# Kernel tuning notes

Hardware: AMD Instinct MI355X
Metric: run time of the kernel (lower is better)

The kernel has to match this reference:

```python
import jax, jax.numpy as jnp
import numpy as np
from jax import lax

DN = ('NHWC', 'HWIO', 'NHWC')

def conv2d_same(x, W, b):
    y = lax.conv_general_dilated(x, W, window_strides=(1, 1), padding='SAME', dimension_numbers=DN)
    return y + b

def maxpool2(x):
    # 2x2 max pool, stride 2, SAME padding (NHWC)
    return lax.reduce_window(x, -jnp.inf, lax.max, (1, 2, 2, 1), (1, 2, 2, 1), 'SAME')

def setup_inputs() -> dict:
    key = jax.random.key(0)
    ks = jax.random.split(key, 6)
    B, H, W, C = 8, 64, 64, 256
    s = 0.05
    return {
        'x': jax.random.normal(ks[0], (B, H, W, C), jnp.float32),
        'Wf': jax.random.normal(ks[1], (3, 3, C, C // 8), jnp.float32) * s,
        'bf': jnp.zeros((C // 8,), jnp.float32),
        'Wg': jax.random.normal(ks[2], (3, 3, C, C // 8), jnp.float32) * s,
        'bg': jnp.zeros((C // 8,), jnp.float32),
        'Wh': jax.random.normal(ks[3], (3, 3, C, C // 2), jnp.float32) * s,
        'bh': jnp.zeros((C // 2,), jnp.float32),
        'Wo': jax.random.normal(ks[4], (1, 1, C // 2, C), jnp.float32) * s,
        'bo': jnp.zeros((C,), jnp.float32),
        'gate': jnp.ones((1,), jnp.float32),
    }

def reference(x, Wf, bf, Wg, bg, Wh, bh, Wo, bo, gate):
    B, H, W, C = x.shape
    f = maxpool2(conv2d_same(x, Wf, bf))            # [B, H/2, W/2, C//8] keys
    g = conv2d_same(x, Wg, bg)                       # [B, H, W, C//8]     queries
    h = maxpool2(conv2d_same(x, Wh, bh))            # [B, H/2, W/2, C//2] values
    N, M = H * W, (H // 2) * (W // 2)
    gq = g.reshape(B, N, C // 8)
    fk = f.reshape(B, M, C // 8)
    hv = h.reshape(B, M, C // 2)
    attn = jax.nn.softmax(jnp.einsum('bnd,bmd->bnm', gq, fk), axis=-1)  # [B, N, M]
    wo = jnp.einsum('bnm,bmv->bnv', attn, hv).reshape(B, H, W, C // 2)
    out = conv2d_same(wo, Wo, bo)                    # [B, H, W, C]
    return x + gate[0] * out
```

## Files before the change

kernel.cpp:

```cpp
#include <hip/hip_runtime.h>
#include <hip/hip_fp16.h>

constexpr int B_  = 8;
constexpr int H_  = 64;
constexpr int W_  = 64;
constexpr int C_  = 256;
constexpr int CG_ = 32;
constexpr int CH_ = 128;
constexpr int NQ_ = 4096;
constexpr int NM_ = 1024;
constexpr int XP_ = 66;

constexpr int GP_ = 1048576;
constexpr int HP_ = 4194304;

constexpr int NWPK_ = 12 * 9 * 8 * 64 * 8;
constexpr int NWOK_ = 16 * 4 * 64 * 8;
constexpr int NXC_  = B_ * XP_ * XP_ * 32;

typedef __attribute__((ext_vector_type(8))) _Float16 half8;
typedef __attribute__((ext_vector_type(4))) _Float16 half4;
typedef __attribute__((ext_vector_type(4))) float    f32x4;

__global__ void prep_all_k(const float* __restrict__ X,
                           const float* __restrict__ Wg, const float* __restrict__ Wf,
                           const float* __restrict__ Wh, const float* __restrict__ Wo,
                           const float* __restrict__ bg, const float* __restrict__ bf,
                           const float* __restrict__ bh,
                           _Float16* __restrict__ Xpad, _Float16* __restrict__ Wpk,
                           _Float16* __restrict__ Wok, float* __restrict__ bc) {
    int i = blockIdx.x * 256 + threadIdx.x;
    if (i < NXC_) {
        int c8 = i & 31;
        int px = i >> 5;
        int xx = px % XP_;
        int t  = px / XP_;
        int yy = t % XP_;
        int b  = t / XP_;
        half8 v = (half8)(_Float16)0.f;
        if (yy >= 1 && yy <= 64 && xx >= 1 && xx <= 64) {
            const float* s = X + (((size_t)(b * 64 + yy - 1) * 64) + (xx - 1)) * 256 + c8 * 8;
            float4 a  = *reinterpret_cast<const float4*>(s);
            float4 b2 = *reinterpret_cast<const float4*>(s + 4);
            v[0] = (_Float16)a.x;  v[1] = (_Float16)a.y;
            v[2] = (_Float16)a.z;  v[3] = (_Float16)a.w;
            v[4] = (_Float16)b2.x; v[5] = (_Float16)b2.y;
            v[6] = (_Float16)b2.z; v[7] = (_Float16)b2.w;
        }
        *reinterpret_cast<half8*>(Xpad + (size_t)i * 8) = v;
        return;
    }
    int iw = i - NXC_;
    if (iw < NWPK_) {
        int j    = iw & 7;
        int lane = (iw >> 3) & 63;
        int ks   = (iw >> 9) & 7;
        int tap  = (iw >> 12) % 9;
        int co16 = iw / 36864;
        int co = co16 * 16 + (lane & 15);
        int kk = tap * 256 + ks * 32 + (lane >> 4) * 8 + j;
        float v;
        if (co < 32)      v = Wg[(size_t)kk * 32  + co];
        else if (co < 64) v = Wf[(size_t)kk * 32  + (co - 32)];
        else              v = Wh[(size_t)kk * 128 + (co - 64)];
        Wpk[iw] = (_Float16)v;
        return;
    }
    int i2 = iw - NWPK_;
    if (i2 < NWOK_) {
        int j    = i2 & 7;
        int lane = (i2 >> 3) & 63;
        int ks   = (i2 >> 9) & 3;
        int co16 = i2 >> 11;
        int co = co16 * 16 + (lane & 15);
        int k  = ks * 32 + (lane >> 4) * 8 + j;
        Wok[i2] = (_Float16)Wo[(size_t)k * 256 + co];
        return;
    }
    int co = i2 - NWOK_;
    if (co < 192)
        bc[co] = (co < 32) ? bg[co] : (co < 64) ? bf[co - 32] : bh[co - 64];
}

__global__ __launch_bounds__(256, 8) void conv_mfma_k(
        const _Float16* __restrict__ Xpad, const _Float16* __restrict__ Wpk,
        const float* __restrict__ bc,
        _Float16* __restrict__ gpart, _Float16* __restrict__ fpart,
        _Float16* __restrict__ hpart) {
    __shared__ char lds[34 * 512];
    int bid = blockIdx.x;
    int lg  = (bid & 7) * 384 + (bid >> 3);
    int ky  = lg % 3;
    int t   = lg / 3;
    int xh  = t & 1;
    int y   = (t >> 1) & 63;
    int b   = t >> 7;
    int tid = threadIdx.x;
    int nw  = tid >> 6;
    int l   = tid & 63;
    int lr  = l & 15;
    int lk  = l >> 4;

    {
        const float4* src = reinterpret_cast<const float4*>(
            Xpad + (((size_t)(b * XP_ + y + ky) * XP_) + xh * 32) * 256);
        for (int c = tid; c < 34 * 32; c += 256) {
            int q = c >> 5;
            float4 v = src[c];
            *reinterpret_cast<float4*>(lds + ((c * 16) ^ ((q & 7) << 4))) = v;
        }
    }
    __syncthreads();

    f32x4 acc[2][3];
#pragma unroll
    for (int mi = 0; mi < 2; ++mi)
#pragma unroll
        for (int nj = 0; nj < 3; ++nj) acc[mi][nj] = (f32x4)0.f;

    int tap0 = ky * 3;
#pragma unroll
    for (int st = 0; st < 24; ++st) {
        int kx = st >> 3, ks = st & 7;
        const _Float16* wp = Wpk +
            ((((size_t)(nw * 3) * 9 + tap0 + kx) * 8 + ks) * 64 + l) * 8;
        half8 w0 = *reinterpret_cast<const half8*>(wp);
        half8 w1 = *reinterpret_cast<const half8*>(wp + 36864);
        half8 w2 = *reinterpret_cast<const half8*>(wp + 73728);
        half8 af[2];
#pragma unroll
        for (int mi = 0; mi < 2; ++mi) {
            int q  = mi * 16 + lr + kx;
            int ad = (q * 512 + ks * 64 + lk * 16) ^ ((q & 7) << 4);
            af[mi] = *reinterpret_cast<const half8*>(lds + ad);
        }
#pragma unroll
        for (int mi = 0; mi < 2; ++mi)
            acc[mi][0] = __builtin_amdgcn_mfma_f32_16x16x32_f16(af[mi], w0, acc[mi][0], 0, 0, 0);
#pragma unroll
        for (int mi = 0; mi < 2; ++mi)
            acc[mi][1] = __builtin_amdgcn_mfma_f32_16x16x32_f16(af[mi], w1, acc[mi][1], 0, 0, 0);
#pragma unroll
        for (int mi = 0; mi < 2; ++mi)
            acc[mi][2] = __builtin_amdgcn_mfma_f32_16x16x32_f16(af[mi], w2, acc[mi][2], 0, 0, 0);
    }

    int pixbase = (b * 64 + y) * 64 + xh * 32;
    bool addb = (ky == 1);
#pragma unroll
    for (int nj = 0; nj < 3; ++nj) {
        int co = nw * 48 + nj * 16 + lr;
        float bias = addb ? bc[co] : 0.f;
#pragma unroll
        for (int mi = 0; mi < 2; ++mi) {
#pragma unroll
            for (int r = 0; r < 4; ++r) {
                int px = mi * 16 + lk * 4 + r;
                float v = acc[mi][nj][r] + bias;
                size_t pix = pixbase + px;
                if (co < 32)
                    gpart[(size_t)ky * GP_ + pix * 32 + co] = (_Float16)(v * 1.44269504f);
                else if (co < 64)
                    fpart[(size_t)ky * GP_ + pix * 32 + (co - 32)] = (_Float16)v;
                else
                    hpart[(size_t)ky * HP_ + pix * 128 + (co - 64)] = (_Float16)v;
            }
        }
    }
}

__global__ __launch_bounds__(256) void pools_k(const _Float16* __restrict__ fp,
                                               const _Float16* __restrict__ hp,
                                               _Float16* __restrict__ Kf,
                                               _Float16* __restrict__ Vt) {
    __shared__ float t[32][33];
    int blk = blockIdx.x;
    int tid = threadIdx.x;
    if (blk < 1024) {
        int i = blk * 256 + tid;
        int c = i & 31;
        int t2 = i >> 5;
        int px = t2 & 31;
        int py = (t2 >> 5) & 31;
        int b  = t2 >> 10;
        size_t base = (((size_t)(b * 64 + py * 2)) * 64 + px * 2) * 32 + c;
        const _Float16* p1 = fp + GP_;
        const _Float16* p2 = fp + 2 * GP_;
        auto val = [&](size_t o) { return (float)fp[o] + (float)p1[o] + (float)p2[o]; };
        float v = fmaxf(fmaxf(val(base), val(base + 32)),
                        fmaxf(val(base + 64 * 32), val(base + 64 * 32 + 32)));
        Kf[i] = (_Float16)v;
        return;
    }
    int bx = blk - 1024;
    int b  = bx >> 7;
    int kt = (bx >> 2) & 31;
    int ct = bx & 3;
    const _Float16* p1 = hp + HP_;
    const _Float16* p2 = hp + 2 * (size_t)HP_;
#pragma unroll
    for (int i = 0; i < 4; ++i) {
        int e = tid + i * 256;
        int px = e >> 5, c = e & 31;
        size_t base = (((size_t)(b * 64 + kt * 2) * 64) + px * 2) * 128 + ct * 32 + c;
        auto val = [&](size_t o) { return (float)hp[o] + (float)p1[o] + (float)p2[o]; };
        float v = fmaxf(fmaxf(val(base), val(base + 128)),
                        fmaxf(val(base + 64 * 128), val(base + 64 * 128 + 128)));
        t[px][c] = v;
    }
    __syncthreads();
#pragma unroll
    for (int i = 0; i < 4; ++i) {
        int e = tid + i * 256;
        int c = e >> 5, px = e & 31;
        Vt[((size_t)b * 128 + ct * 32 + c) * 1024 + kt * 32 + px] = (_Float16)t[px][c];
    }
}

constexpr int PP_ = 72;

__global__ __launch_bounds__(256, 2) void attn_flash_k(
        const _Float16* __restrict__ Qp,
        const _Float16* __restrict__ Kf,
        const _Float16* __restrict__ Vt,
        _Float16* __restrict__ wo) {
    __shared__ _Float16 plds[4][16][PP_];
    __shared__ _Float16 vlds[2][8192];
    int bb  = blockIdx.x >> 6;
    int qt  = blockIdx.x & 63;
    int wid = threadIdx.x >> 6;
    int l   = threadIdx.x & 63;
    int lr  = l & 15;
    int lg  = l >> 4;
    int qbase = qt * 64 + wid * 16;

    const _Float16* gp = Qp + ((size_t)bb * NQ_ + qbase + lr) * 32 + lg * 8;
    half8 bq = *reinterpret_cast<const half8*>(gp);
    bq = bq + *reinterpret_cast<const half8*>(gp + GP_);
    bq = bq + *reinterpret_cast<const half8*>(gp + 2 * GP_);

    const _Float16* Kb = Kf + (size_t)bb * NM_ * 32;
    const _Float16* Vb = Vt + (size_t)bb * 128 * NM_;

    int o0  = wid * 4096 + l * 16;
    int vr0 = o0 >> 7;
    int vc  = (o0 >> 4) & 7;
    int vsw = (vr0 & 7) << 4;
    int lsw = (lr & 7) << 4;

    f32x4 acc[8];
#pragma unroll
    for (int vt = 0; vt < 8; ++vt) acc[vt] = (f32x4)0.f;
    float m_run = -1.0e30f;
    float l_lane = 0.f;

    half8 ak0, ak1, ak2, ak3;
    f32x4 s0, s1, s2, s3;
    half4 ph0, ph1, ph2, ph3;
    float4 vst[4];

#define STAGE_LOAD(T)                                                              \
    {   const _Float16* vp = Vb + (size_t)(T) * 64 + (size_t)vr0 * NM_ + vc * 8;   \
        vst[0] = *reinterpret_cast<const float4*>(vp);                             \
        vst[1] = *reinterpret_cast<const float4*>(vp + 8 * NM_);                   \
        vst[2] = *reinterpret_cast<const float4*>(vp + 16 * NM_);                  \
        vst[3] = *reinterpret_cast<const float4*>(vp + 24 * NM_);                  \
    }

#define STAGE_WRITE(BUF)                                                           \
    {   char* vbp = (char*)vlds[BUF] + (o0 ^ vsw);                                 \
        *reinterpret_cast<float4*>(vbp)        = vst[0];                           \
        *reinterpret_cast<float4*>(vbp + 1024) = vst[1];                           \
        *reinterpret_cast<float4*>(vbp + 2048) = vst[2];                           \
        *reinterpret_cast<float4*>(vbp + 3072) = vst[3];                           \
    }

#define LOADK(T)                                                                   \
    {   const _Float16* kp = Kb + (size_t)(T) * 64 * 32;                           \
        ak0 = *reinterpret_cast<const half8*>(kp + (size_t)(lr)      * 32 + lg*8); \
        ak1 = *reinterpret_cast<const half8*>(kp + (size_t)(16 + lr) * 32 + lg*8); \
        ak2 = *reinterpret_cast<const half8*>(kp + (size_t)(32 + lr) * 32 + lg*8); \
        ak3 = *reinterpret_cast<const half8*>(kp + (size_t)(48 + lr) * 32 + lg*8); \
    }

#define QK()                                                                \
    {   __builtin_amdgcn_s_setprio(1);                                      \
        s0 = __builtin_amdgcn_mfma_f32_16x16x32_f16(ak0, bq, (f32x4)0.f, 0, 0, 0); \
        s1 = __builtin_amdgcn_mfma_f32_16x16x32_f16(ak1, bq, (f32x4)0.f, 0, 0, 0); \
        s2 = __builtin_amdgcn_mfma_f32_16x16x32_f16(ak2, bq, (f32x4)0.f, 0, 0, 0); \
        s3 = __builtin_amdgcn_mfma_f32_16x16x32_f16(ak3, bq, (f32x4)0.f, 0, 0, 0); \
        __builtin_amdgcn_s_setprio(0);                                      \
    }

#define SOFTMAX()                                                           \
    {   float lm = fmaxf(fmaxf(fmaxf(s0[0], s0[1]), fmaxf(s0[2], s0[3])),   \
                         fmaxf(fmaxf(s1[0], s1[1]), fmaxf(s1[2], s1[3])));  \
        lm = fmaxf(lm, fmaxf(fmaxf(fmaxf(s2[0], s2[1]), fmaxf(s2[2], s2[3])), \
                             fmaxf(fmaxf(s3[0], s3[1]), fmaxf(s3[2], s3[3])))); \
        if (__any(lm > m_run + 11.0f)) {                                    \
            float mx = lm;                                                  \
            mx = fmaxf(mx, __shfl_xor(mx, 16, 64));                         \
            mx = fmaxf(mx, __shfl_xor(mx, 32, 64));                         \
            float mnew  = fmaxf(m_run, mx);                                 \
            float alpha = exp2f(m_run - mnew);                              \
            l_lane *= alpha;                                                \
            _Pragma("unroll")                                               \
            for (int r = 0; r < 4; ++r) {                                   \
                float ar = __shfl(alpha, 4 * lg + r, 64);                   \
                _Pragma("unroll")                                           \
                for (int vt = 0; vt < 8; ++vt) acc[vt][r] *= ar;            \
            }                                                               \
            m_run = mnew;                                                   \
        }                                                                   \
        float ps = 0.f;                                                     \
        {   float p0 = exp2f(s0[0]-m_run), p1 = exp2f(s0[1]-m_run);         \
            float p2 = exp2f(s0[2]-m_run), p3 = exp2f(s0[3]-m_run);         \
            ps += (p0+p1)+(p2+p3);                                          \
            ph0[0]=(_Float16)p0; ph0[1]=(_Float16)p1;                       \
            ph0[2]=(_Float16)p2; ph0[3]=(_Float16)p3; }                     \
        {   float p0 = exp2f(s1[0]-m_run), p1 = exp2f(s1[1]-m_run);         \
            float p2 = exp2f(s1[2]-m_run), p3 = exp2f(s1[3]-m_run);         \
            ps += (p0+p1)+(p2+p3);                                          \
            ph1[0]=(_Float16)p0; ph1[1]=(_Float16)p1;                       \
            ph1[2]=(_Float16)p2; ph1[3]=(_Float16)p3; }                     \
        {   float p0 = exp2f(s2[0]-m_run), p1 = exp2f(s2[1]-m_run);         \
            float p2 = exp2f(s2[2]-m_run), p3 = exp2f(s2[3]-m_run);         \
            ps += (p0+p1)+(p2+p3);                                          \
            ph2[0]=(_Float16)p0; ph2[1]=(_Float16)p1;                       \
            ph2[2]=(_Float16)p2; ph2[3]=(_Float16)p3; }                     \
        {   float p0 = exp2f(s3[0]-m_run), p1 = exp2f(s3[1]-m_run);         \
            float p2 = exp2f(s3[2]-m_run), p3 = exp2f(s3[3]-m_run);         \
            ps += (p0+p1)+(p2+p3);                                          \
            ph3[0]=(_Float16)p0; ph3[1]=(_Float16)p1;                       \
            ph3[2]=(_Float16)p2; ph3[3]=(_Float16)p3; }                     \
        l_lane += ps;                                                       \
    }

#define WRITEP()                                                            \
    {   *reinterpret_cast<half4*>(&plds[wid][lr][ 0 + 4*lg]) = ph0;         \
        *reinterpret_cast<half4*>(&plds[wid][lr][16 + 4*lg]) = ph1;         \
        *reinterpret_cast<half4*>(&plds[wid][lr][32 + 4*lg]) = ph2;         \
        *reinterpret_cast<half4*>(&plds[wid][lr][48 + 4*lg]) = ph3;         \
    }

#define PV(BUF)                                                             \
    {   half8 ap0 = *reinterpret_cast<const half8*>(&plds[wid][lr][8*lg]);  \
        half8 ap1 = *reinterpret_cast<const half8*>(&plds[wid][lr][32 + 8*lg]); \
        const char* vbp = (const char*)vlds[BUF];                           \
        __builtin_amdgcn_s_setprio(1);                                      \
        _Pragma("unroll")                                                   \
        for (int vt = 0; vt < 8; ++vt) {                                    \
            int ra = (vt * 16 + lr) * 128;                                  \
            half8 bv = *reinterpret_cast<const half8*>(                     \
                vbp + ((ra + lg * 16) ^ lsw));                              \
            acc[vt] = __builtin_amdgcn_mfma_f32_16x16x32_f16(ap0, bv, acc[vt], 0, 0, 0); \
        }                                                                   \
        _Pragma("unroll")                                                   \
        for (int vt = 0; vt < 8; ++vt) {                                    \
            int ra = (vt * 16 + lr) * 128;                                  \
            half8 bv = *reinterpret_cast<const half8*>(                     \
                vbp + ((ra + (4 + lg) * 16) ^ lsw));                        \
            acc[vt] = __builtin_amdgcn_mfma_f32_16x16x32_f16(ap1, bv, acc[vt], 0, 0, 0); \
        }                                                                   \
        __builtin_amdgcn_s_setprio(0);                                      \
    }

    STAGE_LOAD(0);
    STAGE_WRITE(0);
    LOADK(0);
    __syncthreads();
    QK(); SOFTMAX();

    for (int t = 0; t < 16; ++t) {
        if (t < 15) { STAGE_LOAD(t + 1); LOADK(t + 1); }
        WRITEP();
        PV(t & 1);
        if (t < 15) STAGE_WRITE((t + 1) & 1);
        __syncthreads();
        if (t < 15) { QK(); SOFTMAX(); }
    }

#undef STAGE_LOAD
#undef STAGE_WRITE
#undef LOADK
#undef QK
#undef SOFTMAX
#undef WRITEP
#undef PV

    float lsum = l_lane;
    lsum += __shfl_xor(lsum, 16, 64);
    lsum += __shfl_xor(lsum, 32, 64);
    float inv = 1.f / lsum;
#pragma unroll
    for (int r = 0; r < 4; ++r) {
        float ir = __shfl(inv, 4 * lg + r, 64);
        _Float16* orow = wo + ((size_t)bb * NQ_ + qbase + 4 * lg + r) * 128 + lr;
#pragma unroll
        for (int vt = 0; vt < 8; ++vt) orow[vt * 16] = (_Float16)(acc[vt][r] * ir);
    }
}

__global__ __launch_bounds__(256, 2) void conv1x1_mfma_k(
        const _Float16* __restrict__ wo, const _Float16* __restrict__ Wok,
        const float* __restrict__ bo, const float* __restrict__ X,
        const float* __restrict__ gate, float* __restrict__ out) {
    __shared__ char lds[64 * 256];
    int pix0 = blockIdx.x * 64;
    int tid = threadIdx.x;
    int wq = tid >> 6;
    int l  = tid & 63;
    int lr = l & 15;
    int lg = l >> 4;

    {
        const float4* sp = reinterpret_cast<const float4*>(wo + (size_t)pix0 * 128);
#pragma unroll
        for (int j = 0; j < 4; ++j) {
            int c = tid + j * 256;
            int px = c >> 4;
            *reinterpret_cast<float4*>(lds + ((c * 16) ^ ((px & 7) << 4))) = sp[c];
        }
    }
    __syncthreads();

    f32x4 acc[4][4];
#pragma unroll
    for (int mi = 0; mi < 4; ++mi)
#pragma unroll
        for (int nj = 0; nj < 4; ++nj) acc[mi][nj] = (f32x4)0.f;

#pragma unroll
    for (int ks = 0; ks < 4; ++ks) {
        half8 ap[4];
#pragma unroll
        for (int mi = 0; mi < 4; ++mi) {
            int px = mi * 16 + lr;
            int ad = (px * 256 + ks * 64 + lg * 16) ^ ((px & 7) << 4);
            ap[mi] = *reinterpret_cast<const half8*>(lds + ad);
        }
#pragma unroll
        for (int nj = 0; nj < 4; ++nj) {
            int co16 = wq * 4 + nj;
            half8 bv = *reinterpret_cast<const half8*>(
                Wok + (((size_t)co16 * 4 + ks) * 64 + l) * 8);
#pragma unroll
            for (int mi = 0; mi < 4; ++mi)
                acc[mi][nj] = __builtin_amdgcn_mfma_f32_16x16x32_f16(ap[mi], bv, acc[mi][nj], 0, 0, 0);
        }
    }

    float gt = gate[0];
#pragma unroll
    for (int nj = 0; nj < 4; ++nj) {
        int co = wq * 64 + nj * 16 + lr;
        float bias = bo[co];
#pragma unroll
        for (int mi = 0; mi < 4; ++mi) {
#pragma unroll
            for (int r = 0; r < 4; ++r) {
                size_t o = (size_t)(pix0 + mi * 16 + lg * 4 + r) * 256 + co;
                out[o] = X[o] + gt * (acc[mi][nj][r] + bias);
            }
        }
    }
}

extern "C" void kernel_launch(void* const* d_in, const int* in_sizes, int n_in,
                              void* d_out, int out_size, void* d_ws, size_t ws_size,
                              hipStream_t stream) {
    const float* X    = (const float*)d_in[0];
    const float* Wf   = (const float*)d_in[1];
    const float* bf   = (const float*)d_in[2];
    const float* Wg   = (const float*)d_in[3];
    const float* bg   = (const float*)d_in[4];
    const float* Wh   = (const float*)d_in[5];
    const float* bh   = (const float*)d_in[6];
    const float* Wo   = (const float*)d_in[7];
    const float* bo   = (const float*)d_in[8];
    const float* gate = (const float*)d_in[9];
    float* out = (float*)d_out;

    _Float16* gpart = (_Float16*)d_ws;
    _Float16* fpart = gpart + 3 * (size_t)GP_;
    _Float16* hpart = fpart + 3 * (size_t)GP_;
    _Float16* Kf    = hpart + 3 * (size_t)HP_;
    _Float16* Vt    = Kf + 262144;
    _Float16* Wpk   = Vt + 1048576;
    float*    bc    = (float*)(Wpk + 589824);
    _Float16* Wok   = (_Float16*)(bc + 192);
    _Float16* Xpad  = Wok + 32768;
    _Float16* wobuf = hpart;

    int prep_n = NXC_ + NWPK_ + NWOK_ + 192;
    prep_all_k<<<(prep_n + 255) / 256, 256, 0, stream>>>(
        X, Wg, Wf, Wh, Wo, bg, bf, bh, Xpad, Wpk, Wok, bc);
    conv_mfma_k<<<3 * B_ * 64 * 2, 256, 0, stream>>>(Xpad, Wpk, bc, gpart, fpart, hpart);
    pools_k<<<2048, 256, 0, stream>>>(fpart, hpart, Kf, Vt);
    attn_flash_k<<<B_ * 64, 256, 0, stream>>>(gpart, Kf, Vt, wobuf);
    conv1x1_mfma_k<<<(B_ * NQ_) / 64, 256, 0, stream>>>(wobuf, Wok, bo, X, gate, out);
}
```

Baseline: 118.4 us.

## Process full image row per conv block and prefetch next weight fragments

```diff
diff --git a/kernel.cpp b/kernel.cpp
--- a/kernel.cpp
+++ b/kernel.cpp
@@ -82,82 +82,96 @@
         bc[co] = (co < 32) ? bg[co] : (co < 64) ? bf[co - 32] : bh[co - 64];
 }
 
-__global__ __launch_bounds__(256, 8) void conv_mfma_k(
+__global__ __launch_bounds__(256, 4) void conv_mfma_k(
         const _Float16* __restrict__ Xpad, const _Float16* __restrict__ Wpk,
         const float* __restrict__ bc,
         _Float16* __restrict__ gpart, _Float16* __restrict__ fpart,
         _Float16* __restrict__ hpart) {
-    __shared__ char lds[34 * 512];
+    __shared__ char lds[XP_ * 256 * 2];
     int bid = blockIdx.x;
-    int lg  = (bid & 7) * 384 + (bid >> 3);
+    int lg  = (bid & 7) * 192 + (bid >> 3);
     int ky  = lg % 3;
-    int t   = lg / 3;
-    int xh  = t & 1;
-    int y   = (t >> 1) & 63;
-    int b   = t >> 7;
+    int iy  = lg / 3;
+    int b   = iy >> 6;
+    int y   = iy & 63;
     int tid = threadIdx.x;
-    int nw  = tid >> 6;
+    int wid = tid >> 6;
     int l   = tid & 63;
     int lr  = l & 15;
     int lk  = l >> 4;
 
     {
-        const float4* src = reinterpret_cast<const float4*>(
-            Xpad + (((size_t)(b * XP_ + y + ky) * XP_) + xh * 32) * 256);
-        for (int c = tid; c < 34 * 32; c += 256) {
-            int q = c >> 5;
-            float4 v = src[c];
-            *reinterpret_cast<float4*>(lds + ((c * 16) ^ ((q & 7) << 4))) = v;
+        const float4* sp = reinterpret_cast<const float4*>(
+            Xpad + ((size_t)(b * XP_ + y + ky) * XP_) * 256);
+        float4 vst[8];
+#pragma unroll
+        for (int j = 0; j < 8; ++j) vst[j] = sp[tid + j * 256];
+        float4 tl;
+        if (tid < 64) tl = sp[tid + 2048];
+#pragma unroll
+        for (int j = 0; j < 8; ++j) {
+            int c = tid + j * 256; int px = c >> 5;
+            *reinterpret_cast<float4*>(lds + ((c * 16) ^ ((px & 7) << 4))) = vst[j];
+        }
+        if (tid < 64) {
+            int c = tid + 2048; int px = c >> 5;
+            *reinterpret_cast<float4*>(lds + ((c * 16) ^ ((px & 7) << 4))) = tl;
         }
     }
     __syncthreads();
 
-    f32x4 acc[2][3];
-#pragma unroll
-    for (int mi = 0; mi < 2; ++mi)
+    f32x4 acc[4][3];
+#pragma unroll
+    for (int mi = 0; mi < 4; ++mi)
 #pragma unroll
         for (int nj = 0; nj < 3; ++nj) acc[mi][nj] = (f32x4)0.f;
 
+    auto ldw = [&](int tap, int ks, half8& d0, half8& d1, half8& d2) {
+        const _Float16* p = Wpk + ((((size_t)(wid * 3) * 9 + tap) * 8 + ks) * 64 + l) * 8;
+        d0 = *reinterpret_cast<const half8*>(p);
+        d1 = *reinterpret_cast<const half8*>(p + 36864);
+        d2 = *reinterpret_cast<const half8*>(p + 73728);
+    };
+
     int tap0 = ky * 3;
+    half8 b0, b1, b2, n0, n1, n2;
+    ldw(tap0, 0, b0, b1, b2);
 #pragma unroll
     for (int st = 0; st < 24; ++st) {
         int kx = st >> 3, ks = st & 7;
-        const _Float16* wp = Wpk +
-            ((((size_t)(nw * 3) * 9 + tap0 + kx) * 8 + ks) * 64 + l) * 8;
-        half8 w0 = *reinterpret_cast<const half8*>(wp);
-        half8 w1 = *reinterpret_cast<const half8*>(wp + 36864);
-        half8 w2 = *reinterpret_cast<const half8*>(wp + 73728);
-        half8 af[2];
-#pragma unroll
-        for (int mi = 0; mi < 2; ++mi) {
-            int q  = mi * 16 + lr + kx;
-            int ad = (q * 512 + ks * 64 + lk * 16) ^ ((q & 7) << 4);
+        if (st < 23) ldw(tap0 + ((st + 1) >> 3), (st + 1) & 7, n0, n1, n2);
+        half8 af[4];
+#pragma unroll
+        for (int mi = 0; mi < 4; ++mi) {
+            int px = mi * 16 + lr + kx;
+            int ad = (px * 512 + ks * 64 + lk * 16) ^ ((px & 7) << 4);
             af[mi] = *reinterpret_cast<const half8*>(lds + ad);
         }
 #pragma unroll
-        for (int mi = 0; mi < 2; ++mi)
-            acc[mi][0] = __builtin_amdgcn_mfma_f32_16x16x32_f16(af[mi], w0, acc[mi][0], 0, 0, 0);
-#pragma unroll
-        for (int mi = 0; mi < 2; ++mi)
-            acc[mi][1] = __builtin_amdgcn_mfma_f32_16x16x32_f16(af[mi], w1, acc[mi][1], 0, 0, 0);
-#pragma unroll
-        for (int mi = 0; mi < 2; ++mi)
-            acc[mi][2] = __builtin_amdgcn_mfma_f32_16x16x32_f16(af[mi], w2, acc[mi][2], 0, 0, 0);
-    }
-
-    int pixbase = (b * 64 + y) * 64 + xh * 32;
+        for (int mi = 0; mi < 4; ++mi)
+            acc[mi][0] = __builtin_amdgcn_mfma_f32_16x16x32_f16(af[mi], b0, acc[mi][0], 0, 0, 0);
+#pragma unroll
+        for (int mi = 0; mi < 4; ++mi)
+            acc[mi][1] = __builtin_amdgcn_mfma_f32_16x16x32_f16(af[mi], b1, acc[mi][1], 0, 0, 0);
+#pragma unroll
+        for (int mi = 0; mi < 4; ++mi)
+            acc[mi][2] = __builtin_amdgcn_mfma_f32_16x16x32_f16(af[mi], b2, acc[mi][2], 0, 0, 0);
+        b0 = n0; b1 = n1; b2 = n2;
+    }
+
+    int pixbase = (b * 64 + y) * 64;
     bool addb = (ky == 1);
 #pragma unroll
     for (int nj = 0; nj < 3; ++nj) {
-        int co = nw * 48 + nj * 16 + lr;
+        int co = wid * 48 + nj * 16 + lr;
         float bias = addb ? bc[co] : 0.f;
 #pragma unroll
-        for (int mi = 0; mi < 2; ++mi) {
+        for (int mi = 0; mi < 4; ++mi) {
 #pragma unroll
             for (int r = 0; r < 4; ++r) {
-                int px = mi * 16 + lk * 4 + r;
+                int x = mi * 16 + lk * 4 + r;
                 float v = acc[mi][nj][r] + bias;
-                size_t pix = pixbase + px;
+                size_t pix = pixbase + x;
                 if (co < 32)
                     gpart[(size_t)ky * GP_ + pix * 32 + co] = (_Float16)(v * 1.44269504f);
                 else if (co < 64)
@@ -495,7 +509,7 @@
     int prep_n = NXC_ + NWPK_ + NWOK_ + 192;
     prep_all_k<<<(prep_n + 255) / 256, 256, 0, stream>>>(
         X, Wg, Wf, Wh, Wo, bg, bf, bh, Xpad, Wpk, Wok, bc);
-    conv_mfma_k<<<3 * B_ * 64 * 2, 256, 0, stream>>>(Xpad, Wpk, bc, gpart, fpart, hpart);
+    conv_mfma_k<<<3 * B_ * H_, 256, 0, stream>>>(Xpad, Wpk, bc, gpart, fpart, hpart);
     pools_k<<<2048, 256, 0, stream>>>(fpart, hpart, Kf, Vt);
     attn_flash_k<<<B_ * 64, 256, 0, stream>>>(gpart, Kf, Vt, wobuf);
     conv1x1_mfma_k<<<(B_ * NQ_) / 64, 256, 0, stream>>>(wobuf, Wok, bo, X, gate, out);
```

After: 104.2 us (median of 2 runs). -12.0%, faster.

## Switch 3x3 conv to 32x32x16 MFMA over full-row tiles with weight prefetch

Applied to the files above, without the earlier changes.

```diff
diff --git a/kernel.cpp b/kernel.cpp
--- a/kernel.cpp
+++ b/kernel.cpp
@@ -14,13 +14,14 @@
 constexpr int GP_ = 1048576;
 constexpr int HP_ = 4194304;
 
-constexpr int NWPK_ = 12 * 9 * 8 * 64 * 8;
+constexpr int NWPK_ = 6 * 9 * 16 * 64 * 8;
 constexpr int NWOK_ = 16 * 4 * 64 * 8;
 constexpr int NXC_  = B_ * XP_ * XP_ * 32;
 
-typedef __attribute__((ext_vector_type(8))) _Float16 half8;
-typedef __attribute__((ext_vector_type(4))) _Float16 half4;
-typedef __attribute__((ext_vector_type(4))) float    f32x4;
+typedef __attribute__((ext_vector_type(8)))  _Float16 half8;
+typedef __attribute__((ext_vector_type(4)))  _Float16 half4;
+typedef __attribute__((ext_vector_type(4)))  float    f32x4;
+typedef __attribute__((ext_vector_type(16))) float    f32x16;
 
 __global__ void prep_all_k(const float* __restrict__ X,
                            const float* __restrict__ Wg, const float* __restrict__ Wf,
@@ -54,11 +55,11 @@
     if (iw < NWPK_) {
         int j    = iw & 7;
         int lane = (iw >> 3) & 63;
-        int ks   = (iw >> 9) & 7;
-        int tap  = (iw >> 12) % 9;
-        int co16 = iw / 36864;
-        int co = co16 * 16 + (lane & 15);
-        int kk = tap * 256 + ks * 32 + (lane >> 4) * 8 + j;
+        int ks   = (iw >> 9) & 15;
+        int tap  = (iw >> 13) % 9;
+        int co32 = iw / 73728;
+        int co = co32 * 32 + (lane & 31);
+        int kk = tap * 256 + ks * 16 + (lane >> 5) * 8 + j;
         float v;
         if (co < 32)      v = Wg[(size_t)kk * 32  + co];
         else if (co < 64) v = Wf[(size_t)kk * 32  + (co - 32)];
@@ -82,80 +83,82 @@
         bc[co] = (co < 32) ? bg[co] : (co < 64) ? bf[co - 32] : bh[co - 64];
 }
 
-__global__ __launch_bounds__(256, 8) void conv_mfma_k(
+__global__ __launch_bounds__(192, 3) void conv_mfma_k(
         const _Float16* __restrict__ Xpad, const _Float16* __restrict__ Wpk,
         const float* __restrict__ bc,
         _Float16* __restrict__ gpart, _Float16* __restrict__ fpart,
         _Float16* __restrict__ hpart) {
-    __shared__ char lds[34 * 512];
+    __shared__ char lds[XP_ * 256 * 2];
     int bid = blockIdx.x;
-    int lg  = (bid & 7) * 384 + (bid >> 3);
+    int lg  = (bid & 7) * 192 + (bid >> 3);
     int ky  = lg % 3;
-    int t   = lg / 3;
-    int xh  = t & 1;
-    int y   = (t >> 1) & 63;
-    int b   = t >> 7;
+    int iy  = lg / 3;
+    int b   = iy >> 6;
+    int y   = iy & 63;
     int tid = threadIdx.x;
-    int nw  = tid >> 6;
+    int w   = tid >> 6;
     int l   = tid & 63;
-    int lr  = l & 15;
-    int lk  = l >> 4;
+    int l31 = l & 31;
+    int lh  = l >> 5;
 
     {
-        const float4* src = reinterpret_cast<const float4*>(
-            Xpad + (((size_t)(b * XP_ + y + ky) * XP_) + xh * 32) * 256);
-        for (int c = tid; c < 34 * 32; c += 256) {
-            int q = c >> 5;
-            float4 v = src[c];
-            *reinterpret_cast<float4*>(lds + ((c * 16) ^ ((q & 7) << 4))) = v;
+        const float4* sp = reinterpret_cast<const float4*>(
+            Xpad + ((size_t)(b * XP_ + y + ky) * XP_) * 256);
+        for (int c = tid; c < XP_ * 32; c += 192) {
+            int px = c >> 5;
+            float4 v = sp[c];
+            *reinterpret_cast<float4*>(lds + ((c * 16) ^ ((px & 15) << 4))) = v;
         }
     }
     __syncthreads();
 
-    f32x4 acc[2][3];
+    f32x16 acc[2][2];
 #pragma unroll
     for (int mi = 0; mi < 2; ++mi)
 #pragma unroll
-        for (int nj = 0; nj < 3; ++nj) acc[mi][nj] = (f32x4)0.f;
+        for (int nj = 0; nj < 2; ++nj) acc[mi][nj] = (f32x16)0.f;
 
     int tap0 = ky * 3;
-#pragma unroll
-    for (int st = 0; st < 24; ++st) {
-        int kx = st >> 3, ks = st & 7;
-        const _Float16* wp = Wpk +
-            ((((size_t)(nw * 3) * 9 + tap0 + kx) * 8 + ks) * 64 + l) * 8;
-        half8 w0 = *reinterpret_cast<const half8*>(wp);
-        half8 w1 = *reinterpret_cast<const half8*>(wp + 36864);
-        half8 w2 = *reinterpret_cast<const half8*>(wp + 73728);
+    auto ldw = [&](int s, half8& d0, half8& d1) {
+        const _Float16* p = Wpk +
+            ((((size_t)(w * 2) * 9 + tap0 + (s >> 4)) * 16 + (s & 15)) * 64 + l) * 8;
+        d0 = *reinterpret_cast<const half8*>(p);
+        d1 = *reinterpret_cast<const half8*>(p + 73728);
+    };
+
+    half8 b0, b1, n0, n1;
+    ldw(0, b0, b1);
+#pragma unroll
+    for (int st = 0; st < 48; ++st) {
+        int kx = st >> 4, ks = st & 15;
+        if (st < 47) ldw(st + 1, n0, n1);
         half8 af[2];
 #pragma unroll
         for (int mi = 0; mi < 2; ++mi) {
-            int q  = mi * 16 + lr + kx;
-            int ad = (q * 512 + ks * 64 + lk * 16) ^ ((q & 7) << 4);
+            int px = mi * 32 + l31 + kx;
+            int ad = (px * 512 + ks * 32 + lh * 16) ^ ((px & 15) << 4);
             af[mi] = *reinterpret_cast<const half8*>(lds + ad);
         }
 #pragma unroll
         for (int mi = 0; mi < 2; ++mi)
-            acc[mi][0] = __builtin_amdgcn_mfma_f32_16x16x32_f16(af[mi], w0, acc[mi][0], 0, 0, 0);
+            acc[mi][0] = __builtin_amdgcn_mfma_f32_32x32x16_f16(af[mi], b0, acc[mi][0], 0, 0, 0);
 #pragma unroll
         for (int mi = 0; mi < 2; ++mi)
-            acc[mi][1] = __builtin_amdgcn_mfma_f32_16x16x32_f16(af[mi], w1, acc[mi][1], 0, 0, 0);
-#pragma unroll
-        for (int mi = 0; mi < 2; ++mi)
-            acc[mi][2] = __builtin_amdgcn_mfma_f32_16x16x32_f16(af[mi], w2, acc[mi][2], 0, 0, 0);
-    }
-
-    int pixbase = (b * 64 + y) * 64 + xh * 32;
+            acc[mi][1] = __builtin_amdgcn_mfma_f32_32x32x16_f16(af[mi], b1, acc[mi][1], 0, 0, 0);
+        b0 = n0; b1 = n1;
+    }
+
+    int pixbase = (b * 64 + y) * 64;
     bool addb = (ky == 1);
 #pragma unroll
-    for (int nj = 0; nj < 3; ++nj) {
-        int co = nw * 48 + nj * 16 + lr;
+    for (int nj = 0; nj < 2; ++nj) {
+        int co = (w * 2 + nj) * 32 + l31;
         float bias = addb ? bc[co] : 0.f;
 #pragma unroll
         for (int mi = 0; mi < 2; ++mi) {
 #pragma unroll
-            for (int r = 0; r < 4; ++r) {
-                int px = mi * 16 + lk * 4 + r;
+            for (int r = 0; r < 16; ++r) {
+                int px = mi * 32 + (r & 3) + 8 * (r >> 2) + 4 * lh;
                 float v = acc[mi][nj][r] + bias;
                 size_t pix = pixbase + px;
                 if (co < 32)
@@ -487,7 +490,7 @@
     _Float16* Kf    = hpart + 3 * (size_t)HP_;
     _Float16* Vt    = Kf + 262144;
     _Float16* Wpk   = Vt + 1048576;
-    float*    bc    = (float*)(Wpk + 589824);
+    float*    bc    = (float*)(Wpk + 442368);
     _Float16* Wok   = (_Float16*)(bc + 192);
     _Float16* Xpad  = Wok + 32768;
     _Float16* wobuf = hpart;
@@ -495,7 +498,7 @@
     int prep_n = NXC_ + NWPK_ + NWOK_ + 192;
     prep_all_k<<<(prep_n + 255) / 256, 256, 0, stream>>>(
         X, Wg, Wf, Wh, Wo, bg, bf, bh, Xpad, Wpk, Wok, bc);
-    conv_mfma_k<<<3 * B_ * 64 * 2, 256, 0, stream>>>(Xpad, Wpk, bc, gpart, fpart, hpart);
+    conv_mfma_k<<<3 * B_ * H_, 192, 0, stream>>>(Xpad, Wpk, bc, gpart, fpart, hpart);
     pools_k<<<2048, 256, 0, stream>>>(fpart, hpart, Kf, Vt);
     attn_flash_k<<<B_ * 64, 256, 0, stream>>>(gpart, Kf, Vt, wobuf);
     conv1x1_mfma_k<<<(B_ * NQ_) / 64, 256, 0, stream>>>(wobuf, Wok, bo, X, gate, out);
```

Result: faster. 111.9 us (-5.5%).
